# Kernel optimization log

Hardware: AMD Instinct MI355X
Metric: run time of the kernel (lower is better)

## Reference

```python
import jax, jax.numpy as jnp
import numpy as np

N1, N2, E = 256, 128, 4096

def _conv(x, w, b):
    # NCHW conv, 3x3, padding=1 (SAME), then ReLU
    y = jax.lax.conv_general_dilated(x, w, (1, 1), 'SAME',
                                     dimension_numbers=('NCHW', 'OIHW', 'NCHW'))
    return jax.nn.relu(y + b[None, :, None, None])

def _pool(x):
    return jax.lax.reduce_window(x, -jnp.inf, jax.lax.max,
                                 (1, 1, 2, 2), (1, 1, 2, 2), 'VALID')

def _sage(x, src, dst, wl, bl, wr, n):
    # torch_geometric SAGEConv: out = lin_l(mean_j x_src) + lin_r(x), then L2 normalize
    agg = jax.ops.segment_sum(x[src], dst, num_segments=n)
    cnt = jax.ops.segment_sum(jnp.ones((src.shape[0],), x.dtype), dst, num_segments=n)
    agg = agg / jnp.maximum(cnt, 1.0)[:, None]
    out = agg @ wl.T + bl + x @ wr.T
    return out / jnp.maximum(jnp.linalg.norm(out, axis=-1, keepdims=True), 1e-12)

def _diff_pool(x, adj, s):
    # torch_geometric dense_diff_pool
    s = jax.nn.softmax(s, axis=-1)
    out = jnp.einsum('bnc,bnf->bcf', s, x)
    out_adj = jnp.einsum('bnc,bnm,bmd->bcd', s, adj, s)
    link = adj - jnp.einsum('bnc,bmc->bnm', s, s)
    link_loss = jnp.sqrt(jnp.sum(link * link)) / adj.size
    ent_loss = jnp.mean(jnp.sum(-s * jnp.log(s + 1e-15), axis=-1))
    return out, out_adj, link_loss, ent_loss

def setup_inputs() -> dict:
    key = jax.random.key(0)
    ks = jax.random.split(key, 16)
    rn = lambda k, shape, sc: jax.random.normal(k, shape, jnp.float32) * sc
    inp = {}
    inp['inputs'] = jax.random.normal(ks[0], (1, 5, 512, 512), jnp.float32)
    inp['edge_index'] = jax.random.randint(ks[1], (2, E), 0, N1)
    chans = [(5, 32), (32, 64), (64, 128), (128, 256), (256, 256)]
    for i, (ci, co) in enumerate(chans):
        inp[f'w{i+1}'] = rn(ks[2 + i], (co, ci, 3, 3), 1.0 / np.sqrt(ci * 9))
        inp[f'b{i+1}'] = jnp.zeros((co,), jnp.float32)
    sdims = [(256, 128), (256, 128), (128, 2)]
    for i, (ci, co) in enumerate(sdims):
        inp[f'sage{i+1}_wl'] = rn(ks[7 + 2 * i], (co, ci), 1.0 / np.sqrt(ci))
        inp[f'sage{i+1}_bl'] = jnp.zeros((co,), jnp.float32)
        inp[f'sage{i+1}_wr'] = rn(ks[8 + 2 * i], (co, ci), 1.0 / np.sqrt(ci))
    return inp

def reference(inputs, edge_index, w1, b1, w2, b2, w3, b3, w4, b4, w5, b5,
              sage1_wl, sage1_bl, sage1_wr, sage2_wl, sage2_bl, sage2_wr,
              sage3_wl, sage3_bl, sage3_wr):
    x = _pool(_conv(inputs, w1, b1))
    x = _pool(_conv(x, w2, b2))
    x = _pool(_conv(x, w3, b3))
    x = _pool(_conv(x, w4, b4))
    x = _pool(_conv(x, w5, b5))            # [1,256,16,16]
    org = x.reshape(N1, N1)                # [256 nodes, 256 feats]
    src, dst = edge_index[0], edge_index[1]
    x1 = _sage(org, src, dst, sage1_wl, sage1_bl, sage1_wr, N1)
    s1 = _sage(org, src, dst, sage2_wl, sage2_bl, sage2_wr, N1)
    # dense adjacency (scipy coo->dense sums duplicate edges)
    adj1 = jnp.zeros((N1, N1), jnp.float32).at[src, dst].add(1.0)
    xp, adjp, ll1, el1 = _diff_pool(x1[None], adj1[None], s1[None])
    xp = xp.reshape(N2, N2)
    adjp = adjp.reshape(N2, N2)
    # vectorized form of the per-row in-place argmax binarization loop
    row_max = jnp.max(adjp, axis=1, keepdims=True)
    edge_out = jnp.where(adjp == row_max, 1.0, 0.0)
    # dense_to_sparse of the binarized matrix (one max per row, generic case)
    cols = jnp.argmax(adjp, axis=1)
    ei2 = jnp.stack([jnp.arange(N2), cols])  # [2,128] int
    nodes_out = jnp.tanh(_sage(xp, ei2[0], ei2[1], sage3_wl, sage3_bl, sage3_wr, N2))
    adj2 = jnp.zeros((N2, N2), jnp.float32).at[ei2[0], ei2[1]].add(1.0)
    s2 = jnp.ones((1, N2, 1), jnp.float32)  # softmax over size-1 dim -> ones
    x2, _, ll2, el2 = _diff_pool(nodes_out[None], adj2[None], s2)
    return (x2.reshape(-1), ll1 + ll2, el1 + el2, nodes_out, edge_out, ei2)
```

## Files before the change

### kernel.cpp

```cpp
#include <hip/hip_runtime.h>
#include <hip/hip_bf16.h>
#include <math.h>

#define N_EDGES 4096
#define NN1 256
#define NN2 128

typedef short v8s __attribute__((ext_vector_type(8)));
typedef float v4f __attribute__((ext_vector_type(4)));

__device__ inline unsigned short f2b(float f){
  union { __hip_bfloat16 h; unsigned short u; } cv;
  cv.h = __float2bfloat16(f);
  return cv.u;
}

template<int NT>
__device__ inline float block_sum(float v, float* red, int t){
  red[t] = v; __syncthreads();
  #pragma unroll
  for (int st = NT/2; st > 0; st >>= 1){
    if (t < st) red[t] += red[t+st];
    __syncthreads();
  }
  float r = red[0]; __syncthreads();
  return r;
}
template<int NT>
__device__ inline float block_max(float v, float* red, int t){
  red[t] = v; __syncthreads();
  #pragma unroll
  for (int st = NT/2; st > 0; st >>= 1){
    if (t < st) red[t] = fmaxf(red[t], red[t+st]);
    __syncthreads();
  }
  float r = red[0]; __syncthreads();
  return r;
}
template<int NT>
__device__ inline int block_min_int(int v, int* red, int t){
  red[t] = v; __syncthreads();
  #pragma unroll
  for (int st = NT/2; st > 0; st >>= 1){
    if (t < st) red[t] = min(red[t], red[t+st]);
    __syncthreads();
  }
  int r = red[0]; __syncthreads();
  return r;
}

template<int CHUNKS, int COUT, int CIN, int SSLABS, int BSTR, int OUTF32>
__global__ __launch_bounds__(256) void conv_mfma(
    const unsigned short* __restrict__ in, const unsigned short* __restrict__ wb,
    const float* __restrict__ bias, unsigned short* __restrict__ outb,
    float* __restrict__ outf,
    int in_row, int in_slab, int out_row, int out_slab)
{
  constexpr int CG  = COUT/32;
  constexpr int TJ  = SSLABS*324;
  constexpr int NST = (TJ + 255) / 256;
  __shared__ unsigned short tileb[2][SSLABS*2600];

  const int cg = blockIdx.x % CG, bx = blockIdx.x / CG, by = blockIdx.y;
  const int tid = threadIdx.x, lane = tid & 63, wv = tid >> 6;
  const int cot = wv >> 1, wp = wv & 1;
  const int ml = lane & 15, g = lane >> 4;

  int tsrc[NST], tlds[NST];
  #pragma unroll
  for (int s2 = 0; s2 < NST; ++s2){
    int j = tid + s2*256;
    if (j < TJ){
      int s = j / 324, rem = j - s*324;
      int row = rem / 18, px = rem - row*18;
      tsrc[s2] = s*in_slab + ((by*16 + row)*in_row + bx*16 + px)*8;
      tlds[s2] = s*2600 + (row*18+px)*8;
    } else { tsrc[s2] = -1; tlds[s2] = 0; }
  }
  const int wbase = (cg*32 + cot*16 + ml)*CIN + g*8;

  v4f acc[8];
  #pragma unroll
  for (int t = 0; t < 8; ++t) acc[t] = (v4f){0.f,0.f,0.f,0.f};

  uint4 rt[NST];
  auto LD = [&](int cb){
    int off = cb*SSLABS*in_slab;
    #pragma unroll
    for (int s2 = 0; s2 < NST; ++s2)
      if (tsrc[s2] >= 0) rt[s2] = *(const uint4*)&in[tsrc[s2] + off];
  };
  auto ST = [&](int b){
    #pragma unroll
    for (int s2 = 0; s2 < NST; ++s2)
      if (tsrc[s2] >= 0) *(uint4*)&tileb[b][tlds[s2]] = rt[s2];
  };
  auto COMPUTE = [&](int b, int cb){
    v8s wa[9];
    const int wo = wbase + cb*32;
    #pragma unroll
    for (int k = 0; k < 9; ++k)
      wa[k] = *(const v8s*)&wb[k*COUT*CIN + wo];
    #pragma unroll
    for (int k9 = 0; k9 < 9; ++k9){
      const int ky = k9/3, kx = k9 - 3*(k9/3);
      #pragma unroll
      for (int tt = 0; tt < 8; ++tt){
        int t = wp*8 + tt;
        v8s bfr = *(const v8s*)&tileb[b][g*BSTR + ((t+ky)*18 + kx + ml)*8];
        acc[tt] = __builtin_amdgcn_mfma_f32_16x16x32_bf16(wa[k9], bfr, acc[tt], 0, 0, 0);
      }
    }
  };

  LD(0); ST(0); __syncthreads();
  for (int cb = 0; cb < CHUNKS; ++cb){
    if (cb + 1 < CHUNKS) LD(cb+1);
    COMPUTE(cb & 1, cb);
    if (cb + 1 < CHUNKS){
      ST((cb+1) & 1);
      __syncthreads();
    }
  }

  const int cob = cg*32 + cot*16 + g*4;
  float b4[4] = {bias[cob], bias[cob+1], bias[cob+2], bias[cob+3]};
  #pragma unroll
  for (int tp = 0; tp < 4; ++tp){
    float m[4];
    #pragma unroll
    for (int r = 0; r < 4; ++r){
      float v = fmaxf(acc[2*tp][r], acc[2*tp+1][r]);
      float o = __shfl_xor(v, 1);
      m[r] = fmaxf(fmaxf(v, o) + b4[r], 0.f);
    }
    if ((lane & 1) == 0){
      int gy = by*8 + wp*4 + tp, gx = bx*8 + (ml >> 1);
      if (OUTF32){
        #pragma unroll
        for (int r = 0; r < 4; ++r)
          outf[(cob + r)*256 + gy*16 + gx] = m[r];
      } else {
        unsigned int u0 = (unsigned)f2b(m[0]) | ((unsigned)f2b(m[1]) << 16);
        unsigned int u1 = (unsigned)f2b(m[2]) | ((unsigned)f2b(m[3]) << 16);
        int slabo = cob >> 3, sub = (g & 1)*4;
        size_t idx = (size_t)slabo*out_slab + (size_t)((gy+1)*out_row + gx+1)*8 + sub;
        *(uint2*)(outb + idx) = make_uint2(u0, u1);
      }
    }
  }
}

__global__ __launch_bounds__(256) void prep_kernel(
    const float* __restrict__ src, unsigned short* __restrict__ p0b,
    const float* __restrict__ w1, const float* __restrict__ w2,
    const float* __restrict__ w3, const float* __restrict__ w4,
    const float* __restrict__ w5, unsigned short* __restrict__ wbb,
    const float* __restrict__ a, const float* __restrict__ b2,
    const float* __restrict__ c2, const float* __restrict__ d2,
    float* __restrict__ o, unsigned short* __restrict__ wsb,
    float* __restrict__ adjz)
{
  int b = blockIdx.x, tid = threadIdx.x;
  if (b < 1024){
    int idx = b*256 + tid;
    int y = idx >> 9, x = idx & 511;
    unsigned short v8[8];
    #pragma unroll
    for (int c = 0; c < 5; ++c) v8[c] = f2b(src[c*262144 + y*512 + x]);
    v8[5] = 0; v8[6] = 0; v8[7] = 0;
    *(uint4*)&p0b[((size_t)(y+1)*516 + (x+1))*8] = *(uint4*)v8;
  } else if (b < 1452){
    int j = (b-1024)*256 + tid;
    int co, ci, CO, CIl, CIsrc, dst; const float* w;
    if (j < 1024)      { co=j>>5;        ci=j&31;        w=w1; CIsrc=5;   CO=32;  CIl=32;  dst=0; }
    else if (j < 3072) { int q=j-1024;   co=q>>5;  ci=q&31;  w=w2; CIsrc=32;  CO=64;  CIl=32;  dst=9216; }
    else if (j < 11264){ int q=j-3072;   co=q>>6;  ci=q&63;  w=w3; CIsrc=64;  CO=128; CIl=64;  dst=27648; }
    else if (j < 44032){ int q=j-11264;  co=q>>7;  ci=q&127; w=w4; CIsrc=128; CO=256; CIl=128; dst=101376; }
    else               { int q=j-44032;  co=q>>8;  ci=q&255; w=w5; CIsrc=256; CO=256; CIl=256; dst=396288; }
    #pragma unroll
    for (int k = 0; k < 9; ++k){
      float val = (ci < CIsrc) ? w[(co*CIsrc + ci)*9 + k] : 0.f;
      wbb[dst + (k*CO + co)*CIl + ci] = f2b(val);
    }
  } else if (b < 1964){
    int idx = (b-1452)*256 + tid;
    int m = idx >> 15, rem = idx & 32767, k = rem >> 7, cc = rem & 127;
    const float* sp = (m==0)?a:(m==1)?b2:(m==2)?c2:d2;
    o[m*32768 + k*128 + cc] = sp[cc*256 + k];
  } else {
    int j = (b-1964)*256 + tid;
    const int c0=2056, c1=6184, c2z=10344, c3=14568, c4=18920, ca=35368;
    if (j >= ca) return;
    if (j >= c4){
      int q = j - c4;
      ((float4*)adjz)[q] = make_float4(0.f,0.f,0.f,0.f);
      return;
    }
    int base, P, R, W, per, rem;
    if (j < c0)       { base=0;       P=516; R=514; W=512; per=2056; rem=j; }
    else if (j < c1)  { base=2121792; P=260; R=258; W=256; per=1032; rem=j-c0; }
    else if (j < c2z) { base=4268352; P=132; R=130; W=128; per=520;  rem=j-c1; }
    else if (j < c3)  { base=5366592; P=68;  R=66;  W=64;  per=264;  rem=j-c2z; }
    else              { base=5941056; P=36;  R=34;  W=32;  per=136;  rem=j-c3; }
    int s = rem / per, r2 = rem - s*per;
    int row, px;
    if (r2 < 2*P){ row = (r2 < P) ? 0 : R-1; px = (r2 < P) ? r2 : r2 - P; }
    else { int q = r2 - 2*P; row = 1 + (q >> 1); px = (q & 1) ? (W+1) : 0; }
    *(uint4*)&wsb[(size_t)base + ((size_t)(s*R + row)*P + px)*8] = make_uint4(0,0,0,0);
  }
}

__global__ void build_adj_kernel(const int* __restrict__ ei, float* adj, float* cnt){
  int e = blockIdx.x*256 + threadIdx.x;
  if (e < N_EDGES){
    int s = ei[e], d = ei[N_EDGES + e];
    atomicAdd(&adj[s*NN1 + d], 1.0f);
    atomicAdd(&cnt[d], 1.0f);
  }
}

__global__ __launch_bounds__(128) void sage12_kernel(
    const float* __restrict__ adj, const float* __restrict__ cnt,
    const float* __restrict__ org,
    const float* __restrict__ wl1t, const float* __restrict__ bl1, const float* __restrict__ wr1t,
    const float* __restrict__ wl2t, const float* __restrict__ bl2, const float* __restrict__ wr2t,
    float* __restrict__ x1, float* __restrict__ s_out, float* __restrict__ st,
    float* __restrict__ entpart)
{
  __shared__ float sa[NN1], so[NN1], col[NN1], red[128];
  int n = blockIdx.x, c = threadIdx.x;
  for (int k = c; k < NN1; k += 128){
    col[k] = adj[k*NN1 + n];
    so[k]  = org[n*NN1 + k];
  }
  __syncthreads();
  float a0 = 0.f, a1 = 0.f;
  #pragma unroll 4
  for (int s2 = 0; s2 < NN1; ++s2){
    float av = col[s2];
    a0 += av * org[s2*NN1 + c];
    a1 += av * org[s2*NN1 + c + 128];
  }
  float cd = fmaxf(cnt[n], 1.0f);
  sa[c] = a0 / cd;
  sa[c+128] = a1 / cd;
  __syncthreads();

  float p1 = bl1[c], p2 = bl2[c];
  for (int k = 0; k < NN1; ++k){
    float av = sa[k], ov = so[k];
    p1 += av*wl1t[k*128+c] + ov*wr1t[k*128+c];
    p2 += av*wl2t[k*128+c] + ov*wr2t[k*128+c];
  }
  float n1s = block_sum<128>(p1*p1, red, c);
  x1[n*128 + c] = p1 / fmaxf(sqrtf(n1s), 1e-12f);
  float n2s = block_sum<128>(p2*p2, red, c);
  float p2n = p2 / fmaxf(sqrtf(n2s), 1e-12f);
  float mx = block_max<128>(p2n, red, c);
  float ev = expf(p2n - mx);
  float ssum = block_sum<128>(ev, red, c);
  float sv = ev / ssum;
  s_out[n*128 + c] = sv;
  st[c*NN1 + n] = sv;
  float esum = block_sum<128>(-sv * logf(sv + 1e-15f), red, c);
  if (c == 0) entpart[n] = esum;
}

__global__ __launch_bounds__(256) void fuse1_kernel(
    const float* __restrict__ s, const float* __restrict__ x1,
    const float* __restrict__ adj, const float* __restrict__ st,
    float* __restrict__ xp, float* __restrict__ t, float* __restrict__ linkpart)
{
  __shared__ float sn[128]; __shared__ float red[256];
  int b = blockIdx.x, tid = threadIdx.x;
  if (b < 64){
    int cc = b*2 + (tid >> 7), f = tid & 127;
    float acc = 0.f;
    for (int n = 0; n < NN1; ++n) acc += s[n*128+cc] * x1[n*128+f];
    xp[cc*128+f] = acc;
  } else if (b < 192){
    int n = (b-64)*2 + (tid >> 7), c = tid & 127;
    float acc = 0.f;
    for (int m = 0; m < NN1; ++m){
      float a = adj[n*NN1+m];
      if (a != 0.f) acc += a * s[m*128+c];
    }
    t[n*128+c] = acc;
  } else {
    int n = b - 192, m = tid;
    if (m < 128) sn[m] = s[n*128+m];
    __syncthreads();
    float dot = 0.f;
    for (int c = 0; c < 128; ++c) dot += sn[c]*st[c*NN1 + m];
    float v = adj[n*NN1+m] - dot;
    float part = block_sum<256>(v*v, red, m);
    if (m == 0) linkpart[n] = part;
  }
}

__global__ __launch_bounds__(128) void adjp_bin_kernel(
    const float* __restrict__ s, const float* __restrict__ t,
    float* __restrict__ edge_out, float* __restrict__ ei2_out, int* __restrict__ cols)
{
  __shared__ float scol[NN1]; __shared__ float red[128]; __shared__ int redi[128];
  int cc = blockIdx.x, j = threadIdx.x;
  scol[j]       = s[j*128 + cc];
  scol[j + 128] = s[(j+128)*128 + cc];
  __syncthreads();
  float acc = 0.f;
  for (int n = 0; n < NN1; ++n) acc += scol[n] * t[n*128 + j];
  float mx = block_max<128>(acc, red, j);
  edge_out[cc*128+j] = (acc == mx) ? 1.0f : 0.0f;
  int cand = (acc == mx) ? j : (1 << 30);
  int cmin = block_min_int<128>(cand, redi, j);
  if (j == 0){
    cols[cc] = cmin;
    ei2_out[cc] = (float)cc;
    ei2_out[128 + cc] = (float)cmin;
  }
}

__global__ __launch_bounds__(128) void sage3_kernel(
    const float* __restrict__ xp, const int* __restrict__ cols,
    const float* __restrict__ wl3, const float* __restrict__ bl3,
    const float* __restrict__ wr3, float* __restrict__ nodes_out)
{
  __shared__ int colsl[NN2]; __shared__ float red[128];
  int n = blockIdx.x, f = threadIdx.x;
  colsl[f] = cols[f];
  __syncthreads();
  float acc = 0.f, c = 0.f;
  for (int i = 0; i < NN2; ++i){
    if (colsl[i] == n){ acc += xp[i*128+f]; c += 1.f; }
  }
  float ag = acc / fmaxf(c, 1.f);
  float xv = xp[n*128+f];
  float q0 = block_sum<128>(ag*wl3[f]     + xv*wr3[f],     red, f);
  float q1 = block_sum<128>(ag*wl3[128+f] + xv*wr3[128+f], red, f);
  if (f == 0){
    float p0 = q0 + bl3[0], p1 = q1 + bl3[1];
    float nm = fmaxf(sqrtf(p0*p0 + p1*p1), 1e-12f);
    nodes_out[n*2+0] = tanhf(p0/nm);
    nodes_out[n*2+1] = tanhf(p1/nm);
  }
}

__global__ __launch_bounds__(256) void finalize_kernel(const float* __restrict__ linkpart,
    const float* __restrict__ entpart, float* __restrict__ d_out)
{
  __shared__ float red[256];
  int t = threadIdx.x;
  float ls = block_sum<256>(linkpart[t], red, t);
  float es = block_sum<256>(entpart[t], red, t);
  float v0 = 0.f, v1 = 0.f;
  if (t < 128){ v0 = d_out[4 + t*2 + 0]; v1 = d_out[4 + t*2 + 1]; }
  float s0 = block_sum<256>(v0, red, t);
  float s1 = block_sum<256>(v1, red, t);
  if (t == 0){
    d_out[0] = s0;
    d_out[1] = s1;
    d_out[2] = sqrtf(ls)/65536.0f + sqrtf(16256.0f)/16384.0f;
    d_out[3] = es/256.0f;
  }
}

extern "C" void kernel_launch(void* const* d_in, const int* in_sizes, int n_in,
                              void* d_out_v, int out_size, void* d_ws, size_t ws_size,
                              hipStream_t stream)
{
  (void)in_sizes; (void)n_in; (void)out_size; (void)ws_size;
  const float* input = (const float*)d_in[0];
  const int*   ei    = (const int*)  d_in[1];
  const float* w1 = (const float*)d_in[2];  const float* b1 = (const float*)d_in[3];
  const float* w2 = (const float*)d_in[4];  const float* b2 = (const float*)d_in[5];
  const float* w3 = (const float*)d_in[6];  const float* b3 = (const float*)d_in[7];
  const float* w4 = (const float*)d_in[8];  const float* b4 = (const float*)d_in[9];
  const float* w5 = (const float*)d_in[10]; const float* b5 = (const float*)d_in[11];
  const float* s1wl = (const float*)d_in[12]; const float* s1bl = (const float*)d_in[13];
  const float* s1wr = (const float*)d_in[14];
  const float* s2wl = (const float*)d_in[15]; const float* s2bl = (const float*)d_in[16];
  const float* s2wr = (const float*)d_in[17];
  const float* s3wl = (const float*)d_in[18]; const float* s3bl = (const float*)d_in[19];
  const float* s3wr = (const float*)d_in[20];
  float* d_out = (float*)d_out_v;
  float* ws = (float*)d_ws;

  unsigned short* P0b = (unsigned short*)(ws);
  unsigned short* Pb1 = (unsigned short*)(ws + 1060896);
  unsigned short* Pb2 = (unsigned short*)(ws + 2134176);
  unsigned short* Pb3 = (unsigned short*)(ws + 2683296);
  unsigned short* Pb4 = (unsigned short*)(ws + 2970528);
  unsigned short* wb  = (unsigned short*)(ws + 3127200);
  float* org = ws + 3620256;
  float* wt  = ws + 3685792;
  float* st  = ws + 3816864;
  float* G   = ws + 3849632;

  float* adj1     = G;
  float* cnt      = G + 65536;
  float* x1       = G + 147712;
  float* s        = G + 180480;
  float* t        = G + 213248;
  float* xp       = G + 246016;
  int*   cols     = (int*)(G + 278784);
  float* linkpart = G + 278912;
  float* entpart  = G + 279168;

  prep_kernel<<<dim3(2103), 256, 0, stream>>>(input, P0b, w1, w2, w3, w4, w5, wb,
                                              s1wl, s1wr, s2wl, s2wr, wt,
                                              (unsigned short*)ws, adj1);

  conv_mfma<1,32,32,1,0,0>      <<<dim3(32,32), 256, 0, stream>>>(P0b, wb,        b1, Pb1, nullptr, 516, 2121792, 260, 536640);
  conv_mfma<1,64,32,4,2600,0>   <<<dim3(32,16), 256, 0, stream>>>(Pb1, wb+9216,   b2, Pb2, nullptr, 260, 536640, 132, 137280);
  conv_mfma<2,128,64,4,2600,0>  <<<dim3(32,8),  256, 0, stream>>>(Pb2, wb+27648,  b3, Pb3, nullptr, 132, 137280, 68,  35904);
  conv_mfma<4,256,128,4,2600,0> <<<dim3(32,4),  256, 0, stream>>>(Pb3, wb+101376, b4, Pb4, nullptr, 68,  35904,  36,  9792);
  conv_mfma<8,256,256,4,2600,1> <<<dim3(16,2),  256, 0, stream>>>(Pb4, wb+396288, b5, nullptr, org, 36,  9792,   0,   0);

  build_adj_kernel<<<dim3(16),  256, 0, stream>>>(ei, adj1, cnt);
  sage12_kernel   <<<dim3(256), 128, 0, stream>>>(adj1, cnt, org, wt, s1bl, wt+32768,
                                                  wt+65536, s2bl, wt+98304, x1, s, st, entpart);
  fuse1_kernel    <<<dim3(448), 256, 0, stream>>>(s, x1, adj1, st, xp, t, linkpart);
  adjp_bin_kernel <<<dim3(128), 128, 0, stream>>>(s, t, d_out + 260, d_out + 16644, cols);
  sage3_kernel    <<<dim3(128), 128, 0, stream>>>(xp, cols, s3wl, s3bl, s3wr, d_out + 4);
  finalize_kernel <<<dim3(1),   256, 0, stream>>>(linkpart, entpart, d_out);
}
```

Baseline: 219.8 us.

## Add smaller-tile double-buffered conv kernel for layers 2-5 to raise parallelism

Adds a new conv_mfma2 kernel that uses a 16x4-output spatial tile instead of 16x8, fixes each block to 64 output channels, and double-buffers the shared-memory input tile with register prefetch of the next channel chunk. Layers 2-5 switch to it, which doubles the block count in the spatial dimension. The goal is more blocks on the GPU and overlap of global loads with MFMA work. The cost is extra halo reloads per output, since each tile now carries proportionally more halo rows, and the weight fragments are still read from global memory on every step.

```diff
diff --git a/kernel.cpp b/kernel.cpp
--- a/kernel.cpp
+++ b/kernel.cpp
@@ -146,6 +146,115 @@
         int slabo = cob >> 3, sub = (g & 1)*4;
         size_t idx = (size_t)slabo*out_slab + (size_t)((gy+1)*out_row + gx+1)*8 + sub;
         *(uint2*)(outb + idx) = make_uint2(u0, u1);
+      }
+    }
+  }
+}
+
+template<int CHUNKS, int COUT, int CIN, int OUTF32>
+__global__ __launch_bounds__(256) void conv_mfma2(
+    const unsigned short* __restrict__ in, const unsigned short* __restrict__ wb,
+    const float* __restrict__ bias, unsigned short* __restrict__ outb,
+    float* __restrict__ outf,
+    int in_row, int in_slab, int out_row, int out_slab)
+{
+  constexpr int CG   = COUT/64;
+  constexpr int SSLABS = 4;
+  constexpr int SLST = 1448;
+  constexpr int TJ   = SSLABS*180;
+  constexpr int NST  = (TJ + 255) / 256;
+  __shared__ unsigned short tileb[2][SSLABS*SLST];
+
+  const int cg = blockIdx.x % CG, bx = blockIdx.x / CG, by = blockIdx.y;
+  const int tid = threadIdx.x, lane = tid & 63, wv = tid >> 6;
+  const int p = wv >> 1, wp = wv & 1;
+  const int ml = lane & 15, g = lane >> 4;
+
+  int tsrc[NST], tlds[NST];
+  #pragma unroll
+  for (int s2 = 0; s2 < NST; ++s2){
+    int j = tid + s2*256;
+    if (j < TJ){
+      int s = j / 180, rem = j - s*180;
+      int row = rem / 18, px = rem - row*18;
+      tsrc[s2] = s*in_slab + ((by*8 + row)*in_row + bx*16 + px)*8;
+      tlds[s2] = s*SLST + (row*18+px)*8;
+    } else { tsrc[s2] = -1; tlds[s2] = 0; }
+  }
+  const int wb0 = (cg*64 + (2*p+0)*16 + ml)*CIN + g*8;
+  const int wb1 = (cg*64 + (2*p+1)*16 + ml)*CIN + g*8;
+
+  v4f acc[2][4];
+  #pragma unroll
+  for (int ti = 0; ti < 2; ++ti)
+    #pragma unroll
+    for (int t = 0; t < 4; ++t) acc[ti][t] = (v4f){0.f,0.f,0.f,0.f};
+
+  uint4 rt[NST];
+  auto LD = [&](int cb){
+    int off = cb*SSLABS*in_slab;
+    #pragma unroll
+    for (int s2 = 0; s2 < NST; ++s2)
+      if (tsrc[s2] >= 0) rt[s2] = *(const uint4*)&in[tsrc[s2] + off];
+  };
+  auto ST = [&](int b){
+    #pragma unroll
+    for (int s2 = 0; s2 < NST; ++s2)
+      if (tsrc[s2] >= 0) *(uint4*)&tileb[b][tlds[s2]] = rt[s2];
+  };
+  auto COMPUTE = [&](int b, int cb){
+    const int wo = cb*32;
+    #pragma unroll
+    for (int k9 = 0; k9 < 9; ++k9){
+      const int ky = k9/3, kx = k9 - 3*(k9/3);
+      v8s wa0 = *(const v8s*)&wb[k9*COUT*CIN + wb0 + wo];
+      v8s wa1 = *(const v8s*)&wb[k9*COUT*CIN + wb1 + wo];
+      #pragma unroll
+      for (int tt = 0; tt < 4; ++tt){
+        int t = wp*4 + tt;
+        v8s bfr = *(const v8s*)&tileb[b][g*SLST + ((t+ky)*18 + kx + ml)*8];
+        acc[0][tt] = __builtin_amdgcn_mfma_f32_16x16x32_bf16(wa0, bfr, acc[0][tt], 0, 0, 0);
+        acc[1][tt] = __builtin_amdgcn_mfma_f32_16x16x32_bf16(wa1, bfr, acc[1][tt], 0, 0, 0);
+      }
+    }
+  };
+
+  LD(0); ST(0); __syncthreads();
+  for (int cb = 0; cb < CHUNKS; ++cb){
+    if (cb + 1 < CHUNKS) LD(cb+1);
+    COMPUTE(cb & 1, cb);
+    if (cb + 1 < CHUNKS){
+      ST((cb+1) & 1);
+      __syncthreads();
+    }
+  }
+
+  #pragma unroll
+  for (int ti = 0; ti < 2; ++ti){
+    const int cob = cg*64 + (2*p+ti)*16 + g*4;
+    float b4[4] = {bias[cob], bias[cob+1], bias[cob+2], bias[cob+3]};
+    #pragma unroll
+    for (int tp = 0; tp < 2; ++tp){
+      float m[4];
+      #pragma unroll
+      for (int r = 0; r < 4; ++r){
+        float v = fmaxf(acc[ti][2*tp][r], acc[ti][2*tp+1][r]);
+        float o = __shfl_xor(v, 1);
+        m[r] = fmaxf(fmaxf(v, o) + b4[r], 0.f);
+      }
+      if ((lane & 1) == 0){
+        int gy = by*4 + wp*2 + tp, gx = bx*8 + (ml >> 1);
+        if (OUTF32){
+          #pragma unroll
+          for (int r = 0; r < 4; ++r)
+            outf[(cob + r)*256 + gy*16 + gx] = m[r];
+        } else {
+          unsigned int u0 = (unsigned)f2b(m[0]) | ((unsigned)f2b(m[1]) << 16);
+          unsigned int u1 = (unsigned)f2b(m[2]) | ((unsigned)f2b(m[3]) << 16);
+          int slabo = cob >> 3, sub = (g & 1)*4;
+          size_t idx = (size_t)slabo*out_slab + (size_t)((gy+1)*out_row + gx+1)*8 + sub;
+          *(uint2*)(outb + idx) = make_uint2(u0, u1);
+        }
       }
     }
   }
@@ -411,11 +520,11 @@
                                               s1wl, s1wr, s2wl, s2wr, wt,
                                               (unsigned short*)ws, adj1);
 
-  conv_mfma<1,32,32,1,0,0>      <<<dim3(32,32), 256, 0, stream>>>(P0b, wb,        b1, Pb1, nullptr, 516, 2121792, 260, 536640);
-  conv_mfma<1,64,32,4,2600,0>   <<<dim3(32,16), 256, 0, stream>>>(Pb1, wb+9216,   b2, Pb2, nullptr, 260, 536640, 132, 137280);
-  conv_mfma<2,128,64,4,2600,0>  <<<dim3(32,8),  256, 0, stream>>>(Pb2, wb+27648,  b3, Pb3, nullptr, 132, 137280, 68,  35904);
-  conv_mfma<4,256,128,4,2600,0> <<<dim3(32,4),  256, 0, stream>>>(Pb3, wb+101376, b4, Pb4, nullptr, 68,  35904,  36,  9792);
-  conv_mfma<8,256,256,4,2600,1> <<<dim3(16,2),  256, 0, stream>>>(Pb4, wb+396288, b5, nullptr, org, 36,  9792,   0,   0);
+  conv_mfma<1,32,32,1,0,0>  <<<dim3(32,32), 256, 0, stream>>>(P0b, wb, b1, Pb1, nullptr, 516, 2121792, 260, 536640);
+  conv_mfma2<1,64,32,0>    <<<dim3(16,32), 256, 0, stream>>>(Pb1, wb+9216,   b2, Pb2, nullptr, 260, 536640, 132, 137280);
+  conv_mfma2<2,128,64,0>   <<<dim3(16,16), 256, 0, stream>>>(Pb2, wb+27648,  b3, Pb3, nullptr, 132, 137280, 68,  35904);
+  conv_mfma2<4,256,128,0>  <<<dim3(16,8),  256, 0, stream>>>(Pb3, wb+101376, b4, Pb4, nullptr, 68,  35904,  36,  9792);
+  conv_mfma2<8,256,256,1>  <<<dim3(8,4),   256, 0, stream>>>(Pb4, wb+396288, b5, nullptr, org, 36,  9792,   0,   0);
 
   build_adj_kernel<<<dim3(16),  256, 0, stream>>>(ei, adj1, cnt);
   sage12_kernel   <<<dim3(256), 128, 0, stream>>>(adj1, cnt, org, wt, s1bl, wt+32768,
```

After: 218.7 us. About the same (-0.5%).
